# Performance work log

Measured on AMD Instinct MI355X. Metric: run time of the kernel, lower is better.

The kernel has to match this reference:

```python
import jax, jax.numpy as jnp
import numpy as np

EPSILON = 1e-06
MAXIMUM_AREA_RATIO = 0.3
GRID_HEIGHT = 160.0
CUBE = (25.0, 25.0, 32.0)
FEAT_SCALE = 1.0
GRID_SCALE = 1.0
CRANGE = (-1.0, 0.95)


def setup_inputs() -> dict:
    key = jax.random.key(0)
    k1, k2, k3, k4, k5 = jax.random.split(key, 5)
    B, C, H, W = 2, 256, 96, 320
    L, Wg = 128, 128
    n_layers = int(GRID_HEIGHT // CUBE[2])  # 5
    return {
        "feature": jax.random.normal(k1, (B, C, H, W), dtype=jnp.float32),
        "calib": jax.random.normal(k2, (B, 3, 4), dtype=jnp.float32),
        "grid": jax.random.normal(k3, (L, Wg, 3), dtype=jnp.float32),
        "Wc": jax.random.normal(k4, (C, C * n_layers), dtype=jnp.float32) * 0.02,
        "bc": jax.random.normal(k5, (C,), dtype=jnp.float32) * 0.02,
    }


def _cube_corners(cube):
    l, w, h = cube
    x = np.array([-l / 2, l / 2, l / 2, -l / 2, -l / 2, l / 2, l / 2, -l / 2])
    y = np.array([-w / 2, -w / 2, w / 2, w / 2, -w / 2, -w / 2, w / 2, w / 2])
    z = np.array([0, 0, 0, 0, h, h, h, h])
    return jnp.asarray(np.stack([x, y, z], axis=-1), dtype=jnp.float32)  # (8,3)


def _grid_sample_zeros(img, grd):
    # img: [B,C,H,W]; grd: [B,Hg,Wg,2] normalized coords in [-1,1]
    # bilinear, zero padding, align_corners=False (torch default)
    B, C, H, W = img.shape
    x = ((grd[..., 0] + 1.0) * W - 1.0) * 0.5
    y = ((grd[..., 1] + 1.0) * H - 1.0) * 0.5
    x0f = jnp.floor(x)
    y0f = jnp.floor(y)
    x0 = x0f.astype(jnp.int32)
    y0 = y0f.astype(jnp.int32)
    img_flat = img.reshape(B, C, H * W)

    def gather(xi, yi):
        valid = (xi >= 0) & (xi < W) & (yi >= 0) & (yi < H)
        xc = jnp.clip(xi, 0, W - 1)
        yc = jnp.clip(yi, 0, H - 1)
        idx = (yc * W + xc).reshape(B, 1, -1)
        v = jnp.take_along_axis(img_flat, idx, axis=2)
        v = v.reshape((B, C) + grd.shape[1:-1])
        return v * valid[:, None].astype(img.dtype)

    wx1 = x - x0f
    wx0 = 1.0 - wx1
    wy1 = y - y0f
    wy0 = 1.0 - wy1
    out = (gather(x0, y0) * (wx0 * wy0)[:, None]
           + gather(x0 + 1, y0) * (wx1 * wy0)[:, None]
           + gather(x0, y0 + 1) * (wx0 * wy1)[:, None]
           + gather(x0 + 1, y0 + 1) * (wx1 * wy1)[:, None])
    return out


def reference(feature, calib, grid, Wc, bc):
    B, C, H, W = feature.shape
    L, Wg, _ = grid.shape
    dtype = feature.dtype

    # z-layer offsets: (n_layers, 3) with offset only in z
    z_off = jnp.arange(0.0, GRID_HEIGHT, CUBE[2], dtype=dtype)  # (5,)
    n_layers = z_off.shape[0]
    z_corners = jnp.stack([jnp.zeros_like(z_off), jnp.zeros_like(z_off), z_off], axis=-1)
    offset = _cube_corners(CUBE)  # (8,3)

    # corners3d: (n_layers, L, Wg, 8, 3)
    corners = grid[None] + z_corners[:, None, None, :]  # (n,L,Wg,3)
    corners3d = (corners[:, :, :, None, :] + offset[None, None, None]) / GRID_SCALE

    # project with calib (B,3,4): homogeneous matmul then perspective divide
    hom = jnp.concatenate([corners3d, jnp.ones_like(corners3d[..., :1])], axis=-1)  # (n,L,Wg,8,4)
    pts = jnp.einsum('bij,nlwkj->bnlwki', calib, hom)  # (B,n,L,Wg,8,3)
    img_xy = pts[..., :2] / jnp.maximum(pts[..., 2:3], EPSILON)

    img_size = jnp.array([W, H], dtype=dtype) / FEAT_SCALE
    norm = jnp.clip(2.0 * img_xy / img_size - 1.0, CRANGE[0], CRANGE[1])  # (B,n,L,Wg,8,2)

    box_corners = jnp.concatenate([
        jnp.min(norm[..., 0], axis=-1, keepdims=True),
        jnp.min(norm[..., 1], axis=-1, keepdims=True),
        jnp.max(norm[..., 0], axis=-1, keepdims=True),
        jnp.max(norm[..., 1], axis=-1, keepdims=True),
    ], axis=-1)  # (B,n,L,Wg,4)
    box_corners = box_corners.reshape(B, n_layers, L * Wg, 4)

    area = ((box_corners[..., 2:] - box_corners[..., :2]).prod(axis=-1) * (H * W) + EPSILON)
    area = area[:, None]  # (B,1,n,LWg)
    visible = ((area > EPSILON) & (area < H * W * MAXIMUM_AREA_RATIO)).astype(dtype)

    integral = jnp.cumsum(jnp.cumsum(feature, axis=-1), axis=-2)

    lt = _grid_sample_zeros(integral, box_corners[..., [0, 1]])
    rb = _grid_sample_zeros(integral, box_corners[..., [2, 3]])
    rt = _grid_sample_zeros(integral, box_corners[..., [2, 1]])
    lb = _grid_sample_zeros(integral, box_corners[..., [0, 3]])

    vox = (lt + rb - rt - lb) / area * visible  # (B,C,n,LWg)
    # permute(0,3,1,2) -> (B, LWg, C, n); flatten to (B*LWg, C*n)
    vox = jnp.transpose(vox, (0, 3, 1, 2)).reshape(B * L * Wg, C * n_layers)

    ortho = vox @ Wc.T + bc  # (B*LWg, C)
    ortho = ortho.reshape(B, L, Wg, C)
    ortho = jax.nn.relu(jnp.transpose(ortho, (0, 3, 1, 2)))  # (B,C,L,Wg)
    return ortho
```

## Files before the change

kernel.cpp:

```cpp
#include <hip/hip_runtime.h>
#include <hip/hip_bf16.h>
#include <stdint.h>

#define BB 2
#define CC 256
#define HH 96
#define WW 320
#define NPIX 16384
#define NLAY 5
#define KDIM 1280
#define NDIM 32768
#define NGRP 256
#define BSP 264

typedef float f32x4 __attribute__((ext_vector_type(4)));
typedef float f32x2 __attribute__((ext_vector_type(2)));
typedef __bf16 bf16x8 __attribute__((ext_vector_type(8)));
typedef __bf16 bf16x4 __attribute__((ext_vector_type(4)));

__global__ __launch_bounds__(1024) void k1f(const float* __restrict__ feat,
                                            float* __restrict__ integ,
                                            const float* __restrict__ gridp,
                                            const float* __restrict__ calib,
                                            const float* __restrict__ Wc,
                                            float4* __restrict__ coords,
                                            float* __restrict__ scales,
                                            __bf16* __restrict__ Wbf,
                                            uint8_t* __restrict__ mask8) {
  const int bid = blockIdx.x;
  if (bid < 480) {
    const int vbid = bid * 4 + (threadIdx.x >> 8);
    const int vt = threadIdx.x & 255;
    if (vbid >= 640) {
      int o = (vbid - 640) * 256 + vt;
      int co = o / KDIM;
      int kk = o % KDIM;
      int n = kk >> 8;
      int c = kk & 255;
      Wbf[o] = (__bf16)Wc[co * KDIM + c * NLAY + n];
      return;
    }
    int box = vbid * 256 + vt;
    int pix = box & (NPIX - 1);
    int bn = box >> 14;
    int n = bn % NLAY;
    int b = bn / NLAY;
    const float* cb = calib + b * 12;
    float c00 = cb[0], c01 = cb[1], c02 = cb[2], c03 = cb[3];
    float c10 = cb[4], c11 = cb[5], c12 = cb[6], c13 = cb[7];
    float c20 = cb[8], c21 = cb[9], c22 = cb[10], c23 = cb[11];
    float gx = gridp[pix * 3 + 0], gy = gridp[pix * 3 + 1], gz = gridp[pix * 3 + 2];
    float zoff = 32.0f * (float)n;
    const float ox[8] = {-12.5f, 12.5f, 12.5f, -12.5f, -12.5f, 12.5f, 12.5f, -12.5f};
    const float oy[8] = {-12.5f, -12.5f, 12.5f, 12.5f, -12.5f, -12.5f, 12.5f, 12.5f};
    float xmn = 1e30f, ymn = 1e30f, xmx = -1e30f, ymx = -1e30f;
#pragma unroll
    for (int k = 0; k < 8; ++k) {
      float X = gx + ox[k];
      float Y = gy + oy[k];
      float Z = gz + zoff + ((k >= 4) ? 32.0f : 0.0f);
      float px = c00 * X + c01 * Y + c02 * Z + c03;
      float py = c10 * X + c11 * Y + c12 * Z + c13;
      float pz = c20 * X + c21 * Y + c22 * Z + c23;
      float d = fmaxf(pz, 1e-6f);
      float nx = fminf(fmaxf(2.0f * (px / d) / 320.0f - 1.0f, -1.0f), 0.95f);
      float ny = fminf(fmaxf(2.0f * (py / d) / 96.0f - 1.0f, -1.0f), 0.95f);
      xmn = fminf(xmn, nx); xmx = fmaxf(xmx, nx);
      ymn = fminf(ymn, ny); ymx = fmaxf(ymx, ny);
    }
    float dx = xmx - xmn, dy = ymx - ymn;
    float area = (dx * dy) * 30720.0f + 1e-6f;
    bool vis = (area > 1e-6f) && (area < 9216.0f);
    {
      __shared__ uint32_t kf[16];
      unsigned long long bal = __ballot(vis);
      if ((threadIdx.x & 63) == 0) kf[threadIdx.x >> 6] = (bal != 0ull) ? 1u : 0u;
      __syncthreads();
      if (vt == 0) {
        int vb = threadIdx.x >> 8;
        int vbid2 = bid * 4 + vb;
        int bn2 = vbid2 >> 6;
        int n2 = bn2 % NLAY, b2 = bn2 / NLAY;
        int g0 = b2 * 128 + (vbid2 & 63) * 2;
        mask8[g0 * 5 + n2]       = (uint8_t)(kf[vb * 4 + 0] | kf[vb * 4 + 1]);
        mask8[(g0 + 1) * 5 + n2] = (uint8_t)(kf[vb * 4 + 2] | kf[vb * 4 + 3]);
      }
    }
    float X0 = ((xmn + 1.0f) * 320.0f - 1.0f) * 0.5f;
    float Y0 = ((ymn + 1.0f) * 96.0f - 1.0f) * 0.5f;
    float X1 = ((xmx + 1.0f) * 320.0f - 1.0f) * 0.5f;
    float Y1 = ((ymx + 1.0f) * 96.0f - 1.0f) * 0.5f;
    coords[box] = make_float4(X0, Y0, X1, Y1);
    scales[box] = vis ? 1.0f / area : 0.0f;
    return;
  }
  __shared__ float tile[WW * 33];
  const int t = threadIdx.x;
  const int wave = t >> 6;
  const int lane = t & 63;
  const int kb = bid - 480;
  const int cg = kb & 7;
  const int h = (kb >> 3) % HH;
  const int b = kb / (8 * HH);
  const int c0 = cg * 32;

  {
    const float* fb = feat + (size_t)((b * CC + c0) * HH + h) * WW;
    const size_t crstride = (size_t)HH * WW;
#pragma unroll
    for (int r = 0; r < 3; ++r) {
      int idx = r * 1024 + t;
      if (idx < 2560) {
        int cr = idx / 80;
        int wq = idx - cr * 80;
        f32x4 v = *(const f32x4*)(fb + cr * crstride + wq * 4);
        *(f32x4*)(&tile[cr * WW + wq * 4]) = v;
      }
    }
  }
  __syncthreads();
  const int ca = wave * 2, cbn = wave * 2 + 1;
  float va[5], vb[5];
#pragma unroll
  for (int j = 0; j < 5; ++j) va[j] = tile[ca * WW + lane * 5 + j];
#pragma unroll
  for (int j = 0; j < 5; ++j) vb[j] = tile[cbn * WW + lane * 5 + j];
#pragma unroll
  for (int j = 1; j < 5; ++j) { va[j] += va[j - 1]; vb[j] += vb[j - 1]; }
  float ta = va[4], tb = vb[4];
  float ia = ta, ib = tb;
#pragma unroll
  for (int d = 1; d < 64; d <<= 1) {
    float ua = __shfl_up(ia, d, 64);
    float ub = __shfl_up(ib, d, 64);
    if (lane >= d) { ia += ua; ib += ub; }
  }
  float pa = ia - ta, pb = ib - tb;
#pragma unroll
  for (int j = 0; j < 5; ++j) { va[j] += pa; vb[j] += pb; }
  __syncthreads();
#pragma unroll
  for (int j = 0; j < 5; ++j) {
    int w = lane * 5 + j;
    tile[w * 33 + ca]  = va[j];
    tile[w * 33 + cbn] = vb[j];
  }
  __syncthreads();
  float* dst = integ + (size_t)((b * HH + h) * WW) * CC + cg * 32;
#pragma unroll
  for (int r = 0; r < 3; ++r) {
    int idx = r * 1024 + t;
    if (idx < 2560) {
      int w = idx >> 3;
      int cq = (idx & 7) * 4;
      float4 o = make_float4(tile[w * 33 + cq + 0], tile[w * 33 + cq + 1],
                             tile[w * 33 + cq + 2], tile[w * 33 + cq + 3]);
      *(float4*)(dst + (size_t)w * CC + cq) = o;
    }
  }
}

__global__ __launch_bounds__(256) void k2_scan(float* __restrict__ integ) {
  const int blk = blockIdx.x;
  const int w = blk % WW;
  const int b = blk / WW;
  const int g = threadIdx.x >> 6;
  const int l = threadIdx.x & 63;
  float* base = integ + ((size_t)(b * HH + g * 24) * WW + w) * CC + l * 4;
  const size_t stride = (size_t)WW * CC;
  f32x4 v[24];
#pragma unroll
  for (int i = 0; i < 24; ++i) v[i] = *(const f32x4*)(base + (size_t)i * stride);
#pragma unroll
  for (int i = 1; i < 24; ++i) v[i] += v[i - 1];
  __shared__ f32x4 part[4][64];
  part[g][l] = v[23];
  __syncthreads();
  f32x4 off = {0.f, 0.f, 0.f, 0.f};
#pragma unroll
  for (int gg = 0; gg < 3; ++gg)
    if (gg < g) off += part[gg][l];
#pragma unroll
  for (int i = 0; i < 24; ++i) *(f32x4*)(base + (size_t)i * stride) = v[i] + off;
}

__global__ __launch_bounds__(512) void k46(const __bf16* __restrict__ A,
                                           const float* __restrict__ integ,
                                           const float4* __restrict__ coords,
                                           const float* __restrict__ scales,
                                           const float* __restrict__ bias,
                                           float* __restrict__ out,
                                           const uint8_t* __restrict__ mask8) {
  __shared__ __align__(16) __bf16 Bs[32 * BSP];
  const int g = blockIdx.x;
  const int b = g >> 9;
  const int pix0 = (g & 511) * 32;
  const int gm = b * 128 + (pix0 >> 7);
  const int tid = threadIdx.x;
  const int lane = tid & 63;
  const int wave = tid >> 6;
  const int wm = (wave >> 1) * 64;
  const int wn = (wave & 1) * 16;
  const int r16 = lane & 15;
  const int q4 = lane >> 4;

  int ln[NLAY], nact = 0;
#pragma unroll
  for (int n = 0; n < NLAY; ++n)
    if (mask8[gm * 5 + n]) ln[nact++] = n;

  f32x4 acc[4];
#pragma unroll
  for (int i = 0; i < 4; ++i) acc[i] = f32x4{0.f, 0.f, 0.f, 0.f};

  for (int la = 0; la < nact; ++la) {
    const int n = ln[la];
    const int bn = b * NLAY + n;
    const float* gbase = integ + (size_t)(b * HH) * WW * CC + lane * 4;
#pragma unroll
    for (int u = 0; u < 4; ++u) {
      const int row = wave * 4 + u;
      const int box = (bn << 14) | (pix0 + row);
      bf16x4* dst = (bf16x4*)(&Bs[row * BSP + lane * 4]);
      const float scale = scales[box];
      if (scale == 0.f) {
        *dst = bf16x4{(__bf16)0.f, (__bf16)0.f, (__bf16)0.f, (__bf16)0.f};
        continue;
      }
      const float4 q = coords[box];
      float xw[4]; int xi[4];
      float yw[4]; int yi[4];
      {
        float f0 = floorf(q.x); int i0 = (int)f0; float w1 = q.x - f0;
        xw[0] = (i0 >= 0 && i0 < WW) ? (1.f - w1) : 0.f;
        xw[1] = (i0 + 1 < WW) ? w1 : 0.f;
        xi[0] = min(max(i0, 0), WW - 1); xi[1] = min(max(i0 + 1, 0), WW - 1);
        float f1 = floorf(q.z); int i1 = (int)f1; float v1 = q.z - f1;
        xw[2] = (i1 >= 0 && i1 < WW) ? -(1.f - v1) : 0.f;
        xw[3] = (i1 + 1 < WW) ? -v1 : 0.f;
        xi[2] = min(max(i1, 0), WW - 1); xi[3] = min(max(i1 + 1, 0), WW - 1);
      }
      {
        float f0 = floorf(q.y); int j0 = (int)f0; float w1 = q.y - f0;
        yw[0] = (j0 >= 0 && j0 < HH) ? (1.f - w1) : 0.f;
        yw[1] = (j0 + 1 < HH) ? w1 : 0.f;
        yi[0] = min(max(j0, 0), HH - 1); yi[1] = min(max(j0 + 1, 0), HH - 1);
        float f1 = floorf(q.w); int j1 = (int)f1; float v1 = q.w - f1;
        yw[2] = (j1 >= 0 && j1 < HH) ? -(1.f - v1) : 0.f;
        yw[3] = (j1 + 1 < HH) ? -v1 : 0.f;
        yi[2] = min(max(j1, 0), HH - 1); yi[3] = min(max(j1 + 1, 0), HH - 1);
      }
      f32x4 val = {0.f, 0.f, 0.f, 0.f};
#pragma unroll
      for (int jj = 0; jj < 4; ++jj) {
        if (yw[jj] == 0.f) continue;
        const float* rp = gbase + (size_t)yi[jj] * WW * CC;
        f32x4 rs = {0.f, 0.f, 0.f, 0.f};
#pragma unroll
        for (int ii = 0; ii < 4; ++ii) {
          if (xw[ii] != 0.f) {
            f32x4 v = *(const f32x4*)(rp + (size_t)xi[ii] * CC);
            rs += xw[ii] * v;
          }
        }
        val += yw[jj] * rs;
      }
      val *= scale;
      *dst = bf16x4{(__bf16)val.x, (__bf16)val.y, (__bf16)val.z, (__bf16)val.w};
    }
    __syncthreads();
    const int kbase = n * 256;
#pragma unroll
    for (int kk = 0; kk < 8; ++kk) {
      const int k0 = kbase + kk * 32;
      bf16x8 af[4];
#pragma unroll
      for (int i = 0; i < 4; ++i)
        af[i] = *(const bf16x8*)(A + (size_t)(wm + i * 16 + r16) * KDIM + k0 + q4 * 8);
      bf16x8 bg = *(const bf16x8*)(&Bs[(wn + r16) * BSP + kk * 32 + q4 * 8]);
#pragma unroll
      for (int i = 0; i < 4; ++i)
        acc[i] = __builtin_amdgcn_mfma_f32_16x16x32_bf16(af[i], bg, acc[i], 0, 0, 0);
    }
    __syncthreads();
  }

#pragma unroll
  for (int i = 0; i < 4; ++i) {
    int pix = pix0 + wn + r16;
#pragma unroll
    for (int r = 0; r < 4; ++r) {
      int co = wm + i * 16 + q4 * 4 + r;
      float v = acc[i][r] + bias[co];
      out[(size_t)(b * CC + co) * NPIX + pix] = fmaxf(v, 0.f);
    }
  }
}

extern "C" void kernel_launch(void* const* d_in, const int* in_sizes, int n_in,
                              void* d_out, int out_size, void* d_ws, size_t ws_size,
                              hipStream_t stream) {
  const float* feat  = (const float*)d_in[0];
  const float* calib = (const float*)d_in[1];
  const float* grid  = (const float*)d_in[2];
  const float* Wc    = (const float*)d_in[3];
  const float* bc    = (const float*)d_in[4];
  float* out = (float*)d_out;

  char* ws = (char*)d_ws;
  const size_t SZ_INTEG = (size_t)BB * HH * WW * CC * 4;
  const size_t SZ_VOX   = (size_t)NDIM * KDIM * 2;
  const size_t SZ_WBF   = (size_t)CC * KDIM * 2;
  const size_t SZ_CRD   = (size_t)BB * NLAY * NPIX * 16;
  const size_t SZ_SCL   = (size_t)BB * NLAY * NPIX * 4;
  const size_t SZ_MSK   = (size_t)NGRP * NLAY;
  if (ws_size < SZ_INTEG + SZ_VOX + SZ_WBF + SZ_CRD + SZ_SCL + SZ_MSK) return;

  float*   integ  = (float*)ws;
  __bf16*  Wbf    = (__bf16*)(ws + SZ_INTEG + SZ_VOX);
  float4*  coords = (float4*)(ws + SZ_INTEG + SZ_VOX + SZ_WBF);
  float*   scales = (float*)(ws + SZ_INTEG + SZ_VOX + SZ_WBF + SZ_CRD);
  uint8_t* mask8  = (uint8_t*)(ws + SZ_INTEG + SZ_VOX + SZ_WBF + SZ_CRD + SZ_SCL);

  k1f<<<dim3(BB * HH * 8 + 480), dim3(1024), 0, stream>>>(
      feat, integ, grid, calib, Wc, coords, scales, Wbf, mask8);
  k2_scan<<<dim3(BB * WW), dim3(256), 0, stream>>>(integ);
  k46<<<dim3(NDIM / 32), dim3(512), 0, stream>>>(Wbf, integ, coords, scales, bc, out, mask8);
}
```

Measured before the change: 170.1 us.

## Load features directly, make bilinear gathers branchless, raise k46 occupancy hint

The row-scan kernel now reads each channel row straight from global memory into registers, dropping the shared-memory staging pass and one barrier. The box-filter sampling loop in k46 issues all sixteen gathers without checking for zero weights, trading possible wasted loads for better memory-level parallelism and less divergence. k46's launch bounds now request a minimum of eight blocks per CU, which may force register spilling. The direct loads are strided by five floats per lane, so they are less well coalesced than the old vectorised loads.

```diff
diff --git a/kernel.cpp b/kernel.cpp
--- a/kernel.cpp
+++ b/kernel.cpp
@@ -102,29 +102,15 @@
   const int cg = kb & 7;
   const int h = (kb >> 3) % HH;
   const int b = kb / (8 * HH);
-  const int c0 = cg * 32;
-
-  {
-    const float* fb = feat + (size_t)((b * CC + c0) * HH + h) * WW;
-    const size_t crstride = (size_t)HH * WW;
-#pragma unroll
-    for (int r = 0; r < 3; ++r) {
-      int idx = r * 1024 + t;
-      if (idx < 2560) {
-        int cr = idx / 80;
-        int wq = idx - cr * 80;
-        f32x4 v = *(const f32x4*)(fb + cr * crstride + wq * 4);
-        *(f32x4*)(&tile[cr * WW + wq * 4]) = v;
-      }
-    }
-  }
-  __syncthreads();
-  const int ca = wave * 2, cbn = wave * 2 + 1;
+  const int c0 = cg * 32 + wave * 2;
+  const float* s0 = feat + (size_t)((b * CC + c0) * HH + h) * WW;
+  const float* s1 = s0 + (size_t)HH * WW;
+
   float va[5], vb[5];
 #pragma unroll
-  for (int j = 0; j < 5; ++j) va[j] = tile[ca * WW + lane * 5 + j];
-#pragma unroll
-  for (int j = 0; j < 5; ++j) vb[j] = tile[cbn * WW + lane * 5 + j];
+  for (int j = 0; j < 5; ++j) va[j] = s0[lane * 5 + j];
+#pragma unroll
+  for (int j = 0; j < 5; ++j) vb[j] = s1[lane * 5 + j];
 #pragma unroll
   for (int j = 1; j < 5; ++j) { va[j] += va[j - 1]; vb[j] += vb[j - 1]; }
   float ta = va[4], tb = vb[4];
@@ -138,7 +124,7 @@
   float pa = ia - ta, pb = ib - tb;
 #pragma unroll
   for (int j = 0; j < 5; ++j) { va[j] += pa; vb[j] += pb; }
-  __syncthreads();
+  const int ca = wave * 2, cbn = wave * 2 + 1;
 #pragma unroll
   for (int j = 0; j < 5; ++j) {
     int w = lane * 5 + j;
@@ -146,7 +132,7 @@
     tile[w * 33 + cbn] = vb[j];
   }
   __syncthreads();
-  float* dst = integ + (size_t)((b * HH + h) * WW) * CC + cg * 32;
+  float* dst = integ + (size_t)((b * HH + h) * WW) * CC + (cg * 32);
 #pragma unroll
   for (int r = 0; r < 3; ++r) {
     int idx = r * 1024 + t;
@@ -184,13 +170,13 @@
   for (int i = 0; i < 24; ++i) *(f32x4*)(base + (size_t)i * stride) = v[i] + off;
 }
 
-__global__ __launch_bounds__(512) void k46(const __bf16* __restrict__ A,
-                                           const float* __restrict__ integ,
-                                           const float4* __restrict__ coords,
-                                           const float* __restrict__ scales,
-                                           const float* __restrict__ bias,
-                                           float* __restrict__ out,
-                                           const uint8_t* __restrict__ mask8) {
+__global__ __launch_bounds__(512, 8) void k46(const __bf16* __restrict__ A,
+                                              const float* __restrict__ integ,
+                                              const float4* __restrict__ coords,
+                                              const float* __restrict__ scales,
+                                              const float* __restrict__ bias,
+                                              float* __restrict__ out,
+                                              const uint8_t* __restrict__ mask8) {
   __shared__ __align__(16) __bf16 Bs[32 * BSP];
   const int g = blockIdx.x;
   const int b = g >> 9;
@@ -253,16 +239,11 @@
       f32x4 val = {0.f, 0.f, 0.f, 0.f};
 #pragma unroll
       for (int jj = 0; jj < 4; ++jj) {
-        if (yw[jj] == 0.f) continue;
         const float* rp = gbase + (size_t)yi[jj] * WW * CC;
-        f32x4 rs = {0.f, 0.f, 0.f, 0.f};
-#pragma unroll
-        for (int ii = 0; ii < 4; ++ii) {
-          if (xw[ii] != 0.f) {
-            f32x4 v = *(const f32x4*)(rp + (size_t)xi[ii] * CC);
-            rs += xw[ii] * v;
-          }
-        }
+        f32x4 rs = xw[0] * *(const f32x4*)(rp + (size_t)xi[0] * CC)
+                 + xw[1] * *(const f32x4*)(rp + (size_t)xi[1] * CC)
+                 + xw[2] * *(const f32x4*)(rp + (size_t)xi[2] * CC)
+                 + xw[3] * *(const f32x4*)(rp + (size_t)xi[3] * CC);
         val += yw[jj] * rs;
       }
       val *= scale;
```

New measurement: 179.2 us. 5.4% more time.
